# Kernel tuning notes

Hardware: AMD Instinct MI355X
Metric: run time of the kernel (lower is better)

The kernel has to match this reference:

```python
import jax, jax.numpy as jnp
import numpy as np
import math

N_EMBD = 1024
N_HEAD = 16
HEAD_SIZE = N_EMBD // N_HEAD
LAYER_IDX = 2
LAMBDA_INIT = 0.8 - 0.6 * math.exp(-0.3 * (LAYER_IDX - 1))
LN_EPS = 1e-5
B, T = 4, 1024


def setup_inputs() -> dict:
    key = jax.random.key(0)
    ks = jax.random.split(key, 11)
    s = 0.02  # weight init scale
    return {
        "x": jax.random.normal(ks[0], (B, T, N_EMBD), dtype=jnp.float32),
        "Wq1": jax.random.normal(ks[1], (N_EMBD, N_EMBD), dtype=jnp.float32) * s,
        "Wq2": jax.random.normal(ks[2], (N_EMBD, N_EMBD), dtype=jnp.float32) * s,
        "Wk1": jax.random.normal(ks[3], (N_EMBD, N_EMBD), dtype=jnp.float32) * s,
        "Wk2": jax.random.normal(ks[4], (N_EMBD, N_EMBD), dtype=jnp.float32) * s,
        "Wv": jax.random.normal(ks[5], (N_EMBD, 2 * N_EMBD), dtype=jnp.float32) * s,
        "Wc": jax.random.normal(ks[6], (2 * N_EMBD, N_EMBD), dtype=jnp.float32) * s,
        "lq1": jax.random.normal(ks[7], (N_HEAD, HEAD_SIZE), dtype=jnp.float32) * 0.1,
        "lk1": jax.random.normal(ks[8], (N_HEAD, HEAD_SIZE), dtype=jnp.float32) * 0.1,
        "lq2": jax.random.normal(ks[9], (N_HEAD, HEAD_SIZE), dtype=jnp.float32) * 0.1,
        "lk2": jax.random.normal(ks[10], (N_HEAD, HEAD_SIZE), dtype=jnp.float32) * 0.1,
    }


def reference(x, Wq1, Wq2, Wk1, Wk2, Wv, Wc, lq1, lk1, lq2, lk2):
    Bx, Tx, C = x.shape
    H, hs = N_HEAD, HEAD_SIZE
    scale = 1.0 / math.sqrt(hs)

    # projections -> (B, T, H, d)
    q1 = (x @ Wq1).reshape(Bx, Tx, H, hs)
    q2 = (x @ Wq2).reshape(Bx, Tx, H, hs)
    k1 = (x @ Wk1).reshape(Bx, Tx, H, hs)
    k2 = (x @ Wk2).reshape(Bx, Tx, H, hs)
    v = (x @ Wv).reshape(Bx, Tx, H, 2 * hs)

    # dual score streams (B, H, T, T)
    att1 = jnp.einsum("bqhd,bkhd->bhqk", q1, k1) * scale
    att2 = jnp.einsum("bqhd,bkhd->bhqk", q2, k2) * scale

    causal = jnp.tril(jnp.ones((Tx, Tx), dtype=bool))  # (T, T)
    neg_inf = jnp.float32(-jnp.inf)
    att1 = jnp.where(causal, att1, neg_inf)
    att2 = jnp.where(causal, att2, neg_inf)
    a1 = jax.nn.softmax(att1, axis=-1)
    a2 = jax.nn.softmax(att2, axis=-1)

    # per-head differential lambda
    lam1 = jnp.exp(jnp.sum(lq1 * lk1, axis=-1))  # (H,)
    lam2 = jnp.exp(jnp.sum(lq2 * lk2, axis=-1))  # (H,)
    lam_full = lam1 - lam2 + LAMBDA_INIT  # (H,)

    att = a1 - lam_full[None, :, None, None] * a2  # dropout = identity (eval)

    # PV matmul -> (B, T, H, 2*hs)
    y = jnp.einsum("bhqk,bkhd->bqhd", att, v)

    # subLN over last dim (no affine)
    mu = jnp.mean(y, axis=-1, keepdims=True)
    var = jnp.mean(jnp.square(y - mu), axis=-1, keepdims=True)
    y = (y - mu) / jnp.sqrt(var + LN_EPS)
    y = y * (1.0 - LAMBDA_INIT)

    y = y.reshape(Bx, Tx, 2 * C)
    return y @ Wc  # resid dropout = identity (eval)
```

## Files before the change

### kernel.cpp

```cpp
#include <hip/hip_runtime.h>


#define T_SEQ 1024
#define NH 16
#define DV 128
#define NPROJ 6144
#define KSTR 72

typedef __bf16 bf16_t;
typedef __bf16 bf16x8 __attribute__((ext_vector_type(8)));
typedef __bf16 bf16x4 __attribute__((ext_vector_type(4)));
typedef short s16x4 __attribute__((ext_vector_type(4)));
typedef float f32x4 __attribute__((ext_vector_type(4)));

#define LAMBDA_INIT 0.35550906759096928f
#define ONE_MINUS_LI 0.6444909324090307f
#define LOG2E 1.4426950408889634f
#define RTHR 44.36f

#if __has_builtin(__builtin_amdgcn_mfma_f32_16x16x16_bf16)
#define MFMA16(a, b, c) __builtin_amdgcn_mfma_f32_16x16x16_bf16(a, b, c, 0, 0, 0)
#elif __has_builtin(__builtin_amdgcn_mfma_f32_16x16x16bf16_1k)
#define MFMA16(a, b, c)                                                       \
  __builtin_amdgcn_mfma_f32_16x16x16bf16_1k(                                  \
      __builtin_bit_cast(s16x4, a), __builtin_bit_cast(s16x4, b), c, 0, 0, 0)
#else
#define MFMA16(a, b, c) (c)
#endif

#define GLDS(g, l)                                                            \
  __builtin_amdgcn_global_load_lds(                                           \
      (const __attribute__((address_space(1))) void*)(g),                     \
      (__attribute__((address_space(3))) void*)(l), 16, 0, 0)

static const size_t OFF_WCAT = 0;
static const size_t OFF_XB = OFF_WCAT + (size_t)6144 * 1024 * 2;
static const size_t OFF_WCT = OFF_XB + (size_t)4096 * 1024 * 2;
static const size_t OFF_PROJ = OFF_WCT + (size_t)2048 * 1024 * 2;
static const size_t OFF_VT = OFF_PROJ + (size_t)4096 * 6144 * 2;
static const size_t OFF_YLN = OFF_VT + (size_t)64 * 128 * 1024 * 2;
static const size_t OFF_LAM = OFF_YLN + (size_t)4096 * 2048 * 2;

__global__ void __launch_bounds__(256) cast_x(const float* __restrict__ x,
                                              bf16_t* __restrict__ o) {
  const int i = (blockIdx.x * 256 + threadIdx.x) * 4;
  float4 v = *(const float4*)(x + i);
  bf16x4 r = {(bf16_t)v.x, (bf16_t)v.y, (bf16_t)v.z, (bf16_t)v.w};
  *(bf16x4*)(o + i) = r;
}

__device__ __forceinline__ void tcast_body(const float* __restrict__ W,
                                           bf16_t* __restrict__ Wt, int K,
                                           int N, int row0) {
  __shared__ float tile[32][33];
  const int k0 = blockIdx.x * 32, n0 = blockIdx.y * 32;
  const int tx = threadIdx.x & 31, ty = threadIdx.x >> 5;
#pragma unroll
  for (int i = 0; i < 32; i += 8)
    tile[ty + i][tx] = W[(long)(k0 + ty + i) * N + n0 + tx];
  __syncthreads();
#pragma unroll
  for (int i = 0; i < 32; i += 8)
    Wt[(long)(row0 + n0 + ty + i) * K + k0 + tx] = (bf16_t)tile[tx][ty + i];
}

__global__ void __launch_bounds__(256) tcast_w(const float* __restrict__ W,
                                               bf16_t* __restrict__ Wt, int K,
                                               int N, int row0) {
  tcast_body(W, Wt, K, N, row0);
}

__global__ void __launch_bounds__(256) tcast_w4(const float* __restrict__ W0,
                                                const float* __restrict__ W1,
                                                const float* __restrict__ W2,
                                                const float* __restrict__ W3,
                                                bf16_t* __restrict__ Wt) {
  const float* Ws[4] = {W0, W1, W2, W3};
  tcast_body(Ws[blockIdx.z], Wt, 1024, 1024, blockIdx.z * 1024);
}

__global__ void lam_kernel(const float* __restrict__ lq1,
                           const float* __restrict__ lk1,
                           const float* __restrict__ lq2,
                           const float* __restrict__ lk2,
                           float* __restrict__ lam) {
  const int h = threadIdx.x;
  if (h < NH) {
    float d1 = 0.f, d2 = 0.f;
    for (int i = 0; i < 64; ++i) {
      d1 += lq1[h * 64 + i] * lk1[h * 64 + i];
      d2 += lq2[h * 64 + i] * lk2[h * 64 + i];
    }
    lam[h] = expf(d1) - expf(d2) + LAMBDA_INIT;
  }
}

#define BM 128
#define BN 128
#define BK 32

template <typename OutT>
__global__ void __launch_bounds__(256) gemm_bt(const bf16_t* __restrict__ A,
                                               const bf16_t* __restrict__ Bt,
                                               OutT* __restrict__ C, int M,
                                               int N, int K) {
  __shared__ __align__(16) bf16_t As[BM * BK];
  __shared__ __align__(16) bf16_t Bs[BN * BK];
  const int tid = threadIdx.x;
  const int w = tid >> 6;
  const int lane = tid & 63;
  const int quad = lane >> 4, l16 = lane & 15;
  const int m0 = blockIdx.y * BM, n0 = blockIdx.x * BN;
  const int wm = (w >> 1) * 64, wn = (w & 1) * 64;
  const int srow = tid >> 2;
  const int scol = (tid & 3) * 8;

  const bf16_t* Ag0 = A + (long)(m0 + srow) * K + scol;
  const bf16_t* Ag1 = Ag0 + (long)64 * K;
  const bf16_t* Bg0 = Bt + (long)(n0 + srow) * K + scol;
  const bf16_t* Bg1 = Bg0 + (long)64 * K;
  bf16_t* lA0 = As + tid * 8;
  bf16_t* lA1 = As + 2048 + tid * 8;
  bf16_t* lB0 = Bs + tid * 8;
  bf16_t* lB1 = Bs + 2048 + tid * 8;

  f32x4 acc[4][4] = {};

  for (int k0 = 0; k0 < K; k0 += BK) {
    GLDS(Ag0 + k0, lA0);
    GLDS(Ag1 + k0, lA1);
    GLDS(Bg0 + k0, lB0);
    GLDS(Bg1 + k0, lB1);
    __syncthreads();
    bf16x8 af[4], bfr[4];
#pragma unroll
    for (int t = 0; t < 4; ++t) {
      af[t] = *(const bf16x8*)(As + (wm + t * 16 + l16) * BK + quad * 8);
      bfr[t] = *(const bf16x8*)(Bs + (wn + t * 16 + l16) * BK + quad * 8);
    }
#pragma unroll
    for (int mt = 0; mt < 4; ++mt)
#pragma unroll
      for (int nt = 0; nt < 4; ++nt)
        acc[mt][nt] = __builtin_amdgcn_mfma_f32_16x16x32_bf16(
            af[mt], bfr[nt], acc[mt][nt], 0, 0, 0);
    __syncthreads();
  }

#pragma unroll
  for (int mt = 0; mt < 4; ++mt)
#pragma unroll
    for (int nt = 0; nt < 4; ++nt) {
      const int col = n0 + wn + nt * 16 + l16;
#pragma unroll
      for (int i = 0; i < 4; ++i) {
        const int row = m0 + wm + mt * 16 + quad * 4 + i;
        C[(long)row * N + col] = (OutT)acc[mt][nt][i];
      }
    }
}

__global__ void __launch_bounds__(256) transpose_v(const bf16_t* __restrict__ proj,
                                                   bf16_t* __restrict__ vt) {
  __shared__ bf16_t tile[32][34];
  const int bh = blockIdx.z;
  const int b = bh >> 4, h = bh & 15;
  const int t0 = blockIdx.x * 32, d0 = blockIdx.y * 32;
  const int tx = threadIdx.x & 31, ty = threadIdx.x >> 5;
  const bf16_t* src = proj + (long)(b * T_SEQ) * NPROJ + 4096 + h * 128;
#pragma unroll
  for (int i = 0; i < 32; i += 8)
    tile[ty + i][tx] = src[(long)(t0 + ty + i) * NPROJ + d0 + tx];
  __syncthreads();
  bf16_t* dst = vt + ((long)(b * NH + h) * DV) * T_SEQ;
#pragma unroll
  for (int i = 0; i < 32; i += 8)
    dst[(long)(d0 + ty + i) * T_SEQ + t0 + tx] = tile[tx][ty + i];
}

__global__ void __launch_bounds__(256) attn_kernel(const bf16_t* __restrict__ proj,
                                                   const bf16_t* __restrict__ vt,
                                                   const float* __restrict__ lamp,
                                                   bf16_t* __restrict__ yln) {
  const int x = blockIdx.x;
  const int qblk = 15 - (x >> 6);
  const int bh = x & 63;
  const int b = bh >> 4, h = bh & 15;
  const int tid = threadIdx.x;
  const int w = tid >> 6, lane = tid & 63;
  const int quad = lane >> 4, l16 = lane & 15;
  const long bT = (long)b * T_SEQ;

  __shared__ __align__(16) bf16_t Ks1[64 * KSTR];
  __shared__ __align__(16) bf16_t Ks2[64 * KSTR];
  __shared__ __align__(16) bf16_t Vs[DV * KSTR];

  const bf16_t* gK1 =
      proj + (bT + (tid >> 3)) * (long)NPROJ + h * 64 + 2048 + (tid & 7) * 8;
  const bf16_t* gK2 = gK1 + 1024;
  const bf16_t* vbase = vt + ((long)(b * NH + h) * DV) * T_SEQ;
  const bf16_t* gV = vbase + (long)(tid >> 3) * T_SEQ + (tid & 7) * 8;
  const int kw0 = (tid >> 3) * KSTR + (tid & 7) * 8;

  const float sc = 0.125f * LOG2E;
  const float lam = lamp[h];

  const int q0 = qblk * 64 + w * 16;
  const int qg = q0 + l16;

  const bf16_t* qrow = proj + (bT + qg) * (long)NPROJ + h * 64;
  bf16x8 aq1[2], aq2[2];
  aq1[0] = *(const bf16x8*)(qrow + quad * 8);
  aq1[1] = *(const bf16x8*)(qrow + 32 + quad * 8);
  aq2[0] = *(const bf16x8*)(qrow + 1024 + quad * 8);
  aq2[1] = *(const bf16x8*)(qrow + 1024 + 32 + quad * 8);

  f32x4 O1[8] = {}, O2[8] = {};
  float m1 = -3.0e38f, m2 = -3.0e38f, l1 = 0.f, l2 = 0.f;

  const int kend_blk = qblk * 64 + 64;
  const int kend_w = q0 + 16;

  const bf16x4 one4 = {(bf16_t)1.0f, (bf16_t)1.0f, (bf16_t)1.0f, (bf16_t)1.0f};

  bf16x8 rK1[2], rK2[2], rV[4];
  rK1[0] = *(const bf16x8*)(gK1);
  rK1[1] = *(const bf16x8*)(gK1 + (long)32 * NPROJ);
  rK2[0] = *(const bf16x8*)(gK2);
  rK2[1] = *(const bf16x8*)(gK2 + (long)32 * NPROJ);
#pragma unroll
  for (int j = 0; j < 4; ++j)
    rV[j] = *(const bf16x8*)(gV + (long)(32 * j) * T_SEQ);

  for (int kt = 0; kt < kend_blk; kt += 64) {
    *(bf16x8*)(Ks1 + kw0) = rK1[0];
    *(bf16x8*)(Ks1 + kw0 + 32 * KSTR) = rK1[1];
    *(bf16x8*)(Ks2 + kw0) = rK2[0];
    *(bf16x8*)(Ks2 + kw0 + 32 * KSTR) = rK2[1];
#pragma unroll
    for (int j = 0; j < 4; ++j)
      *(bf16x8*)(Vs + kw0 + j * 32 * KSTR) = rV[j];
    __syncthreads();

    if (kt + 64 < kend_blk) {
      const long ko = (long)(kt + 64) * NPROJ;
      rK1[0] = *(const bf16x8*)(gK1 + ko);
      rK1[1] = *(const bf16x8*)(gK1 + ko + (long)32 * NPROJ);
      rK2[0] = *(const bf16x8*)(gK2 + ko);
      rK2[1] = *(const bf16x8*)(gK2 + ko + (long)32 * NPROJ);
#pragma unroll
      for (int j = 0; j < 4; ++j)
        rV[j] = *(const bf16x8*)(gV + kt + 64 + (long)(32 * j) * T_SEQ);
    }

    if (kt < kend_w) {
      f32x4 s1[4], s2[4];
#pragma unroll
      for (int c = 0; c < 4; ++c) {
        const bf16_t* kr1 = Ks1 + (c * 16 + l16) * KSTR;
        const bf16_t* kr2 = Ks2 + (c * 16 + l16) * KSTR;
        bf16x8 ka0 = *(const bf16x8*)(kr1 + quad * 8);
        bf16x8 ka1 = *(const bf16x8*)(kr1 + 32 + quad * 8);
        f32x4 z = {};
        z = __builtin_amdgcn_mfma_f32_16x16x32_bf16(ka0, aq1[0], z, 0, 0, 0);
        z = __builtin_amdgcn_mfma_f32_16x16x32_bf16(ka1, aq1[1], z, 0, 0, 0);
        s1[c] = z;
        bf16x8 kb0 = *(const bf16x8*)(kr2 + quad * 8);
        bf16x8 kb1 = *(const bf16x8*)(kr2 + 32 + quad * 8);
        f32x4 z2 = {};
        z2 = __builtin_amdgcn_mfma_f32_16x16x32_bf16(kb0, aq2[0], z2, 0, 0, 0);
        z2 = __builtin_amdgcn_mfma_f32_16x16x32_bf16(kb1, aq2[1], z2, 0, 0, 0);
        s2[c] = z2;
      }
      const bool need_mask = (kt + 63 > q0);
      if (need_mask) {
#pragma unroll
        for (int c = 0; c < 4; ++c)
#pragma unroll
          for (int i = 0; i < 4; ++i) {
            const int key = kt + c * 16 + quad * 4 + i;
            if (key > qg) {
              s1[c][i] = -1e30f;
              s2[c][i] = -1e30f;
            }
          }
      }
      float t1[4], t2[4];
#pragma unroll
      for (int c = 0; c < 4; ++c) {
        t1[c] = fmaxf(fmaxf(s1[c][0], s1[c][1]), fmaxf(s1[c][2], s1[c][3]));
        t2[c] = fmaxf(fmaxf(s2[c][0], s2[c][1]), fmaxf(s2[c][2], s2[c][3]));
      }
      float mx1 = fmaxf(fmaxf(t1[0], t1[1]), fmaxf(t1[2], t1[3]));
      float mx2 = fmaxf(fmaxf(t2[0], t2[1]), fmaxf(t2[2], t2[3]));
      mx1 = fmaxf(mx1, __shfl_xor(mx1, 16));
      mx1 = fmaxf(mx1, __shfl_xor(mx1, 32));
      mx2 = fmaxf(mx2, __shfl_xor(mx2, 16));
      mx2 = fmaxf(mx2, __shfl_xor(mx2, 32));
      if (!__all((mx1 <= m1 + RTHR) && (mx2 <= m2 + RTHR))) {
        const float mn1 = fmaxf(m1, mx1), mn2 = fmaxf(m2, mx2);
        const float al1 = exp2f((m1 - mn1) * sc);
        const float al2 = exp2f((m2 - mn2) * sc);
        m1 = mn1;
        m2 = mn2;
#pragma unroll
        for (int f = 0; f < 8; ++f)
#pragma unroll
          for (int i = 0; i < 4; ++i) {
            O1[f][i] *= al1;
            O2[f][i] *= al2;
          }
        l1 *= al1;
        l2 *= al2;
      }
      const float ms1 = m1 * sc, ms2 = m2 * sc;
      bf16x4 pc1[4], pc2[4];
#pragma unroll
      for (int c = 0; c < 4; ++c)
#pragma unroll
        for (int i = 0; i < 4; ++i) {
          pc1[c][i] = (bf16_t)exp2f(fmaf(s1[c][i], sc, -ms1));
          pc2[c][i] = (bf16_t)exp2f(fmaf(s2[c][i], sc, -ms2));
        }
      f32x4 la1 = {}, la2 = {};
#pragma unroll
      for (int c = 0; c < 4; ++c) {
        la1 = MFMA16(one4, pc1[c], la1);
        la2 = MFMA16(one4, pc2[c], la2);
#pragma unroll
        for (int f = 0; f < 8; ++f) {
          bf16x4 va =
              *(const bf16x4*)(Vs + (f * 16 + l16) * KSTR + c * 16 + quad * 4);
          O1[f] = MFMA16(va, pc1[c], O1[f]);
          O2[f] = MFMA16(va, pc2[c], O2[f]);
        }
      }
      l1 += la1[0];
      l2 += la2[0];
    }
    __syncthreads();
  }

  const float inv1 = 1.0f / l1, inv2 = lam / l2;
  float sm = 0.f, sq = 0.f;
#pragma unroll
  for (int f = 0; f < 8; ++f)
#pragma unroll
    for (int i = 0; i < 4; ++i) {
      float y = O1[f][i] * inv1 - O2[f][i] * inv2;
      O1[f][i] = y;
      sm += y;
      sq += y * y;
    }
  sm += __shfl_xor(sm, 16);
  sm += __shfl_xor(sm, 32);
  sq += __shfl_xor(sq, 16);
  sq += __shfl_xor(sq, 32);
  const float mu = sm * (1.0f / 128.0f);
  const float var = sq * (1.0f / 128.0f) - mu * mu;
  const float rs = rsqrtf(var + 1e-5f) * ONE_MINUS_LI;
  bf16_t* dst = yln + (bT + qg) * (long)2048 + h * 128 + quad * 4;
#pragma unroll
  for (int f = 0; f < 8; ++f) {
    bf16x4 o = {(bf16_t)((O1[f][0] - mu) * rs), (bf16_t)((O1[f][1] - mu) * rs),
                (bf16_t)((O1[f][2] - mu) * rs), (bf16_t)((O1[f][3] - mu) * rs)};
    *(bf16x4*)(dst + f * 16) = o;
  }
}

extern "C" void kernel_launch(void* const* d_in, const int* in_sizes, int n_in,
                              void* d_out, int out_size, void* d_ws,
                              size_t ws_size, hipStream_t stream) {
  const float* x = (const float*)d_in[0];
  const float* Wq1 = (const float*)d_in[1];
  const float* Wq2 = (const float*)d_in[2];
  const float* Wk1 = (const float*)d_in[3];
  const float* Wk2 = (const float*)d_in[4];
  const float* Wv = (const float*)d_in[5];
  const float* Wc = (const float*)d_in[6];
  const float* lq1 = (const float*)d_in[7];
  const float* lk1 = (const float*)d_in[8];
  const float* lq2 = (const float*)d_in[9];
  const float* lk2 = (const float*)d_in[10];
  float* out = (float*)d_out;

  char* ws = (char*)d_ws;
  bf16_t* wcat = (bf16_t*)(ws + OFF_WCAT);
  bf16_t* xb = (bf16_t*)(ws + OFF_XB);
  bf16_t* wct = (bf16_t*)(ws + OFF_WCT);
  bf16_t* projb = (bf16_t*)(ws + OFF_PROJ);
  bf16_t* vtb = (bf16_t*)(ws + OFF_VT);
  bf16_t* ylnb = (bf16_t*)(ws + OFF_YLN);
  float* lamp = (float*)(ws + OFF_LAM);

  cast_x<<<4096, 256, 0, stream>>>(x, xb);
  tcast_w4<<<dim3(32, 32, 4), 256, 0, stream>>>(Wq1, Wq2, Wk1, Wk2, wcat);
  tcast_w<<<dim3(32, 64), 256, 0, stream>>>(Wv, wcat, 1024, 2048, 4096);
  tcast_w<<<dim3(64, 32), 256, 0, stream>>>(Wc, wct, 2048, 1024, 0);
  lam_kernel<<<1, 64, 0, stream>>>(lq1, lk1, lq2, lk2, lamp);

  gemm_bt<bf16_t><<<dim3(48, 32), 256, 0, stream>>>(xb, wcat, projb, 4096, 6144, 1024);
  transpose_v<<<dim3(32, 4, 64), 256, 0, stream>>>(projb, vtb);
  attn_kernel<<<dim3(1024), 256, 0, stream>>>(projb, vtb, lamp, ylnb);
  gemm_bt<float><<<dim3(8, 32), 256, 0, stream>>>(ylnb, wct, out, 4096, 1024, 2048);
}
```

Baseline: 334.3 us.

## Drop LDS staging in attention; single-wave blocks read K/V directly from global

The attention kernel now runs one 64-thread wave per block instead of four waves sharing LDS tiles. Each wave loads K and V fragments straight from global memory into registers. The block index is remapped so heads are grouped per XCD and share L2, and the wave stops at its own causal limit rather than the block's. To allow 16-byte V loads that split into two MFMA operands, transpose_v writes V^T with keys interleaved in that order. This removes LDS traffic, barriers and idle waves on the diagonal, at the cost of more global/L2 loads, since each wave re-reads K/V without sharing.

```diff
diff --git a/kernel.cpp b/kernel.cpp
--- a/kernel.cpp
+++ b/kernel.cpp
@@ -5,7 +5,6 @@
 #define NH 16
 #define DV 128
 #define NPROJ 6144
-#define KSTR 72
 
 typedef __bf16 bf16_t;
 typedef __bf16 bf16x8 __attribute__((ext_vector_type(8)));
@@ -172,39 +171,36 @@
   for (int i = 0; i < 32; i += 8)
     tile[ty + i][tx] = src[(long)(t0 + ty + i) * NPROJ + d0 + tx];
   __syncthreads();
-  bf16_t* dst = vt + ((long)(b * NH + h) * DV) * T_SEQ;
-#pragma unroll
-  for (int i = 0; i < 32; i += 8)
-    dst[(long)(d0 + ty + i) * T_SEQ + t0 + tx] = tile[tx][ty + i];
-}
-
-__global__ void __launch_bounds__(256) attn_kernel(const bf16_t* __restrict__ proj,
-                                                   const bf16_t* __restrict__ vt,
-                                                   const float* __restrict__ lamp,
-                                                   bf16_t* __restrict__ yln) {
+  const int d_loc = threadIdx.x >> 3;
+  const int g = threadIdx.x & 7;
+  const int s = g >> 2, qd = g & 3;
+  const int tl = s * 16 + qd * 4;
+  bf16x4 o = {tile[tl + 0][d_loc], tile[tl + 1][d_loc], tile[tl + 2][d_loc],
+              tile[tl + 3][d_loc]};
+  bf16_t* dst = vt + (long)bh * (DV * T_SEQ) + (long)(d0 + d_loc) * T_SEQ;
+  *(bf16x4*)(dst + t0 + qd * 8 + s * 4) = o;
+}
+
+__global__ void __launch_bounds__(64, 3) attn_kernel(const bf16_t* __restrict__ proj,
+                                                     const bf16_t* __restrict__ vt,
+                                                     const float* __restrict__ lamp,
+                                                     bf16_t* __restrict__ yln) {
   const int x = blockIdx.x;
-  const int qblk = 15 - (x >> 6);
-  const int bh = x & 63;
+  const int xcd = x & 7;
+  const int u = x >> 3;
+  const int p2 = u >> 7, r = u & 127;
+  const int qi = r >> 3;
+  const int bhl = p2 * 2 + ((r >> 2) & 1);
+  const int w = r & 3;
+  const int qblk = 15 - qi;
+  const int bh = (bhl << 3) | xcd;
   const int b = bh >> 4, h = bh & 15;
-  const int tid = threadIdx.x;
-  const int w = tid >> 6, lane = tid & 63;
+  const int lane = threadIdx.x;
   const int quad = lane >> 4, l16 = lane & 15;
   const long bT = (long)b * T_SEQ;
 
-  __shared__ __align__(16) bf16_t Ks1[64 * KSTR];
-  __shared__ __align__(16) bf16_t Ks2[64 * KSTR];
-  __shared__ __align__(16) bf16_t Vs[DV * KSTR];
-
-  const bf16_t* gK1 =
-      proj + (bT + (tid >> 3)) * (long)NPROJ + h * 64 + 2048 + (tid & 7) * 8;
-  const bf16_t* gK2 = gK1 + 1024;
-  const bf16_t* vbase = vt + ((long)(b * NH + h) * DV) * T_SEQ;
-  const bf16_t* gV = vbase + (long)(tid >> 3) * T_SEQ + (tid & 7) * 8;
-  const int kw0 = (tid >> 3) * KSTR + (tid & 7) * 8;
-
   const float sc = 0.125f * LOG2E;
   const float lam = lamp[h];
-
   const int q0 = qblk * 64 + w * 16;
   const int qg = q0 + l16;
 
@@ -215,130 +211,104 @@
   aq2[0] = *(const bf16x8*)(qrow + 1024 + quad * 8);
   aq2[1] = *(const bf16x8*)(qrow + 1024 + 32 + quad * 8);
 
+  const bf16_t* kb = proj + (bT + l16) * (long)NPROJ + h * 64 + 2048 + quad * 8;
+  const bf16_t* vb = vt + (long)bh * (DV * T_SEQ) + (long)l16 * T_SEQ + quad * 8;
+
   f32x4 O1[8] = {}, O2[8] = {};
   float m1 = -3.0e38f, m2 = -3.0e38f, l1 = 0.f, l2 = 0.f;
-
-  const int kend_blk = qblk * 64 + 64;
-  const int kend_w = q0 + 16;
-
   const bf16x4 one4 = {(bf16_t)1.0f, (bf16_t)1.0f, (bf16_t)1.0f, (bf16_t)1.0f};
 
-  bf16x8 rK1[2], rK2[2], rV[4];
-  rK1[0] = *(const bf16x8*)(gK1);
-  rK1[1] = *(const bf16x8*)(gK1 + (long)32 * NPROJ);
-  rK2[0] = *(const bf16x8*)(gK2);
-  rK2[1] = *(const bf16x8*)(gK2 + (long)32 * NPROJ);
-#pragma unroll
-  for (int j = 0; j < 4; ++j)
-    rV[j] = *(const bf16x8*)(gV + (long)(32 * j) * T_SEQ);
-
-  for (int kt = 0; kt < kend_blk; kt += 64) {
-    *(bf16x8*)(Ks1 + kw0) = rK1[0];
-    *(bf16x8*)(Ks1 + kw0 + 32 * KSTR) = rK1[1];
-    *(bf16x8*)(Ks2 + kw0) = rK2[0];
-    *(bf16x8*)(Ks2 + kw0 + 32 * KSTR) = rK2[1];
-#pragma unroll
-    for (int j = 0; j < 4; ++j)
-      *(bf16x8*)(Vs + kw0 + j * 32 * KSTR) = rV[j];
-    __syncthreads();
-
-    if (kt + 64 < kend_blk) {
-      const long ko = (long)(kt + 64) * NPROJ;
-      rK1[0] = *(const bf16x8*)(gK1 + ko);
-      rK1[1] = *(const bf16x8*)(gK1 + ko + (long)32 * NPROJ);
-      rK2[0] = *(const bf16x8*)(gK2 + ko);
-      rK2[1] = *(const bf16x8*)(gK2 + ko + (long)32 * NPROJ);
-#pragma unroll
-      for (int j = 0; j < 4; ++j)
-        rV[j] = *(const bf16x8*)(gV + kt + 64 + (long)(32 * j) * T_SEQ);
-    }
-
-    if (kt < kend_w) {
-      f32x4 s1[4], s2[4];
-#pragma unroll
-      for (int c = 0; c < 4; ++c) {
-        const bf16_t* kr1 = Ks1 + (c * 16 + l16) * KSTR;
-        const bf16_t* kr2 = Ks2 + (c * 16 + l16) * KSTR;
-        bf16x8 ka0 = *(const bf16x8*)(kr1 + quad * 8);
-        bf16x8 ka1 = *(const bf16x8*)(kr1 + 32 + quad * 8);
-        f32x4 z = {};
-        z = __builtin_amdgcn_mfma_f32_16x16x32_bf16(ka0, aq1[0], z, 0, 0, 0);
-        z = __builtin_amdgcn_mfma_f32_16x16x32_bf16(ka1, aq1[1], z, 0, 0, 0);
-        s1[c] = z;
-        bf16x8 kb0 = *(const bf16x8*)(kr2 + quad * 8);
-        bf16x8 kb1 = *(const bf16x8*)(kr2 + 32 + quad * 8);
-        f32x4 z2 = {};
-        z2 = __builtin_amdgcn_mfma_f32_16x16x32_bf16(kb0, aq2[0], z2, 0, 0, 0);
-        z2 = __builtin_amdgcn_mfma_f32_16x16x32_bf16(kb1, aq2[1], z2, 0, 0, 0);
-        s2[c] = z2;
+  const int kend = q0 + 16;
+  for (int kt = 0; kt < kend; kt += 64) {
+    f32x4 s1[4], s2[4];
+#pragma unroll
+    for (int c = 0; c < 4; ++c) {
+      const bf16_t* kp = kb + (long)(kt + c * 16) * NPROJ;
+      bf16x8 ka0 = *(const bf16x8*)(kp);
+      bf16x8 ka1 = *(const bf16x8*)(kp + 32);
+      bf16x8 kb0 = *(const bf16x8*)(kp + 1024);
+      bf16x8 kb1 = *(const bf16x8*)(kp + 1056);
+      f32x4 z = {};
+      z = __builtin_amdgcn_mfma_f32_16x16x32_bf16(ka0, aq1[0], z, 0, 0, 0);
+      z = __builtin_amdgcn_mfma_f32_16x16x32_bf16(ka1, aq1[1], z, 0, 0, 0);
+      s1[c] = z;
+      f32x4 z2 = {};
+      z2 = __builtin_amdgcn_mfma_f32_16x16x32_bf16(kb0, aq2[0], z2, 0, 0, 0);
+      z2 = __builtin_amdgcn_mfma_f32_16x16x32_bf16(kb1, aq2[1], z2, 0, 0, 0);
+      s2[c] = z2;
+    }
+    const bool need_mask = (kt + 63 > q0);
+    if (need_mask) {
+#pragma unroll
+      for (int c = 0; c < 4; ++c)
+#pragma unroll
+        for (int i = 0; i < 4; ++i) {
+          const int key = kt + c * 16 + quad * 4 + i;
+          if (key > qg) {
+            s1[c][i] = -1e30f;
+            s2[c][i] = -1e30f;
+          }
+        }
+    }
+    float t1[4], t2[4];
+#pragma unroll
+    for (int c = 0; c < 4; ++c) {
+      t1[c] = fmaxf(fmaxf(s1[c][0], s1[c][1]), fmaxf(s1[c][2], s1[c][3]));
+      t2[c] = fmaxf(fmaxf(s2[c][0], s2[c][1]), fmaxf(s2[c][2], s2[c][3]));
+    }
+    float mx1 = fmaxf(fmaxf(t1[0], t1[1]), fmaxf(t1[2], t1[3]));
+    float mx2 = fmaxf(fmaxf(t2[0], t2[1]), fmaxf(t2[2], t2[3]));
+    mx1 = fmaxf(mx1, __shfl_xor(mx1, 16));
+    mx1 = fmaxf(mx1, __shfl_xor(mx1, 32));
+    mx2 = fmaxf(mx2, __shfl_xor(mx2, 16));
+    mx2 = fmaxf(mx2, __shfl_xor(mx2, 32));
+    if (!__all((mx1 <= m1 + RTHR) && (mx2 <= m2 + RTHR))) {
+      const float mn1 = fmaxf(m1, mx1), mn2 = fmaxf(m2, mx2);
+      const float al1 = exp2f((m1 - mn1) * sc);
+      const float al2 = exp2f((m2 - mn2) * sc);
+      m1 = mn1;
+      m2 = mn2;
+#pragma unroll
+      for (int f = 0; f < 8; ++f)
+#pragma unroll
+        for (int i = 0; i < 4; ++i) {
+          O1[f][i] *= al1;
+          O2[f][i] *= al2;
+        }
+      l1 *= al1;
+      l2 *= al2;
+    }
+    const float ms1 = m1 * sc, ms2 = m2 * sc;
+    bf16x4 pc1[4], pc2[4];
+#pragma unroll
+    for (int c = 0; c < 4; ++c)
+#pragma unroll
+      for (int i = 0; i < 4; ++i) {
+        pc1[c][i] = (bf16_t)exp2f(fmaf(s1[c][i], sc, -ms1));
+        pc2[c][i] = (bf16_t)exp2f(fmaf(s2[c][i], sc, -ms2));
       }
-      const bool need_mask = (kt + 63 > q0);
-      if (need_mask) {
-#pragma unroll
-        for (int c = 0; c < 4; ++c)
-#pragma unroll
-          for (int i = 0; i < 4; ++i) {
-            const int key = kt + c * 16 + quad * 4 + i;
-            if (key > qg) {
-              s1[c][i] = -1e30f;
-              s2[c][i] = -1e30f;
-            }
-          }
+    f32x4 la1 = {}, la2 = {};
+#pragma unroll
+    for (int c = 0; c < 4; ++c) {
+      la1 = MFMA16(one4, pc1[c], la1);
+      la2 = MFMA16(one4, pc2[c], la2);
+    }
+#pragma unroll
+    for (int cp = 0; cp < 2; ++cp) {
+      const bf16_t* vp = vb + kt + cp * 32;
+#pragma unroll
+      for (int f = 0; f < 8; ++f) {
+        bf16x8 va = *(const bf16x8*)(vp + (long)f * 16 * T_SEQ);
+        bf16x4 lo = __builtin_shufflevector(va, va, 0, 1, 2, 3);
+        bf16x4 hi = __builtin_shufflevector(va, va, 4, 5, 6, 7);
+        O1[f] = MFMA16(lo, pc1[2 * cp], O1[f]);
+        O2[f] = MFMA16(lo, pc2[2 * cp], O2[f]);
+        O1[f] = MFMA16(hi, pc1[2 * cp + 1], O1[f]);
+        O2[f] = MFMA16(hi, pc2[2 * cp + 1], O2[f]);
       }
-      float t1[4], t2[4];
-#pragma unroll
-      for (int c = 0; c < 4; ++c) {
-        t1[c] = fmaxf(fmaxf(s1[c][0], s1[c][1]), fmaxf(s1[c][2], s1[c][3]));
-        t2[c] = fmaxf(fmaxf(s2[c][0], s2[c][1]), fmaxf(s2[c][2], s2[c][3]));
-      }
-      float mx1 = fmaxf(fmaxf(t1[0], t1[1]), fmaxf(t1[2], t1[3]));
-      float mx2 = fmaxf(fmaxf(t2[0], t2[1]), fmaxf(t2[2], t2[3]));
-      mx1 = fmaxf(mx1, __shfl_xor(mx1, 16));
-      mx1 = fmaxf(mx1, __shfl_xor(mx1, 32));
-      mx2 = fmaxf(mx2, __shfl_xor(mx2, 16));
-      mx2 = fmaxf(mx2, __shfl_xor(mx2, 32));
-      if (!__all((mx1 <= m1 + RTHR) && (mx2 <= m2 + RTHR))) {
-        const float mn1 = fmaxf(m1, mx1), mn2 = fmaxf(m2, mx2);
-        const float al1 = exp2f((m1 - mn1) * sc);
-        const float al2 = exp2f((m2 - mn2) * sc);
-        m1 = mn1;
-        m2 = mn2;
-#pragma unroll
-        for (int f = 0; f < 8; ++f)
-#pragma unroll
-          for (int i = 0; i < 4; ++i) {
-            O1[f][i] *= al1;
-            O2[f][i] *= al2;
-          }
-        l1 *= al1;
-        l2 *= al2;
-      }
-      const float ms1 = m1 * sc, ms2 = m2 * sc;
-      bf16x4 pc1[4], pc2[4];
-#pragma unroll
-      for (int c = 0; c < 4; ++c)
-#pragma unroll
-        for (int i = 0; i < 4; ++i) {
-          pc1[c][i] = (bf16_t)exp2f(fmaf(s1[c][i], sc, -ms1));
-          pc2[c][i] = (bf16_t)exp2f(fmaf(s2[c][i], sc, -ms2));
-        }
-      f32x4 la1 = {}, la2 = {};
-#pragma unroll
-      for (int c = 0; c < 4; ++c) {
-        la1 = MFMA16(one4, pc1[c], la1);
-        la2 = MFMA16(one4, pc2[c], la2);
-#pragma unroll
-        for (int f = 0; f < 8; ++f) {
-          bf16x4 va =
-              *(const bf16x4*)(Vs + (f * 16 + l16) * KSTR + c * 16 + quad * 4);
-          O1[f] = MFMA16(va, pc1[c], O1[f]);
-          O2[f] = MFMA16(va, pc2[c], O2[f]);
-        }
-      }
-      l1 += la1[0];
-      l2 += la2[0];
-    }
-    __syncthreads();
+    }
+    l1 += la1[0];
+    l2 += la2[0];
   }
 
   const float inv1 = 1.0f / l1, inv2 = lam / l2;
@@ -401,6 +371,6 @@
 
   gemm_bt<bf16_t><<<dim3(48, 32), 256, 0, stream>>>(xb, wcat, projb, 4096, 6144, 1024);
   transpose_v<<<dim3(32, 4, 64), 256, 0, stream>>>(projb, vtb);
-  attn_kernel<<<dim3(1024), 256, 0, stream>>>(projb, vtb, lamp, ylnb);
+  attn_kernel<<<dim3(4096), 64, 0, stream>>>(projb, vtb, lamp, ylnb);
   gemm_bt<float><<<dim3(8, 32), 256, 0, stream>>>(ylnb, wct, out, 4096, 1024, 2048);
 }
```

Measured after the change: 397.0 us. +18.7%, slower.

## Split dual attention streams into separate blocks, add combine kernel and narrower output GEMM

Applied to the files above, without the earlier changes.

The attention kernel now computes each softmax stream (q1/k1 and q2/k2) in its own block, doubling the grid to 2048 blocks. Each block writes a normalized fp16 partial output. A new combine kernel applies lambda, the subLN and the scale, reusing the workspace regions of yln and wcat. The final projection uses a new 64-wide N tile GEMM, which launches twice as many blocks. This raises parallelism and lowers per-block register pressure, at the cost of V tiles being loaded twice, fp16 round trips through memory and an extra kernel launch.

```diff
diff --git a/kernel.cpp b/kernel.cpp
--- a/kernel.cpp
+++ b/kernel.cpp
@@ -10,6 +10,9 @@
 typedef __bf16 bf16_t;
 typedef __bf16 bf16x8 __attribute__((ext_vector_type(8)));
 typedef __bf16 bf16x4 __attribute__((ext_vector_type(4)));
+typedef __bf16 bf16x2 __attribute__((ext_vector_type(2)));
+typedef _Float16 f16x4 __attribute__((ext_vector_type(4)));
+typedef _Float16 f16x2 __attribute__((ext_vector_type(2)));
 typedef short s16x4 __attribute__((ext_vector_type(4)));
 typedef float f32x4 __attribute__((ext_vector_type(4)));
 
@@ -160,6 +163,65 @@
     }
 }
 
+template <typename OutT>
+__global__ void __launch_bounds__(256) gemm_bt_n64(const bf16_t* __restrict__ A,
+                                                   const bf16_t* __restrict__ Bt,
+                                                   OutT* __restrict__ C, int M,
+                                                   int N, int K) {
+  __shared__ __align__(16) bf16_t As[BM * BK];
+  __shared__ __align__(16) bf16_t Bs[64 * BK];
+  const int tid = threadIdx.x;
+  const int w = tid >> 6;
+  const int lane = tid & 63;
+  const int quad = lane >> 4, l16 = lane & 15;
+  const int m0 = blockIdx.y * BM, n0 = blockIdx.x * 64;
+  const int wm = (w >> 1) * 64, wn = (w & 1) * 32;
+  const int srow = tid >> 2;
+  const int scol = (tid & 3) * 8;
+
+  const bf16_t* Ag0 = A + (long)(m0 + srow) * K + scol;
+  const bf16_t* Ag1 = Ag0 + (long)64 * K;
+  const bf16_t* Bg0 = Bt + (long)(n0 + srow) * K + scol;
+  bf16_t* lA0 = As + tid * 8;
+  bf16_t* lA1 = As + 2048 + tid * 8;
+  bf16_t* lB0 = Bs + tid * 8;
+
+  f32x4 acc[4][2] = {};
+
+  for (int k0 = 0; k0 < K; k0 += BK) {
+    GLDS(Ag0 + k0, lA0);
+    GLDS(Ag1 + k0, lA1);
+    GLDS(Bg0 + k0, lB0);
+    __syncthreads();
+    bf16x8 af[4], bfr[2];
+#pragma unroll
+    for (int t = 0; t < 4; ++t)
+      af[t] = *(const bf16x8*)(As + (wm + t * 16 + l16) * BK + quad * 8);
+#pragma unroll
+    for (int t = 0; t < 2; ++t)
+      bfr[t] = *(const bf16x8*)(Bs + (wn + t * 16 + l16) * BK + quad * 8);
+#pragma unroll
+    for (int mt = 0; mt < 4; ++mt)
+#pragma unroll
+      for (int nt = 0; nt < 2; ++nt)
+        acc[mt][nt] = __builtin_amdgcn_mfma_f32_16x16x32_bf16(
+            af[mt], bfr[nt], acc[mt][nt], 0, 0, 0);
+    __syncthreads();
+  }
+
+#pragma unroll
+  for (int mt = 0; mt < 4; ++mt)
+#pragma unroll
+    for (int nt = 0; nt < 2; ++nt) {
+      const int col = n0 + wn + nt * 16 + l16;
+#pragma unroll
+      for (int i = 0; i < 4; ++i) {
+        const int row = m0 + wm + mt * 16 + quad * 4 + i;
+        C[(long)row * N + col] = (OutT)acc[mt][nt][i];
+      }
+    }
+}
+
 __global__ void __launch_bounds__(256) transpose_v(const bf16_t* __restrict__ proj,
                                                    bf16_t* __restrict__ vt) {
   __shared__ bf16_t tile[32][34];
@@ -172,7 +234,7 @@
   for (int i = 0; i < 32; i += 8)
     tile[ty + i][tx] = src[(long)(t0 + ty + i) * NPROJ + d0 + tx];
   __syncthreads();
-  bf16_t* dst = vt + ((long)(b * NH + h) * DV) * T_SEQ;
+  bf16_t* dst = vt + ((long)bh * DV) * T_SEQ;
 #pragma unroll
   for (int i = 0; i < 32; i += 8)
     dst[(long)(d0 + ty + i) * T_SEQ + t0 + tx] = tile[tx][ty + i];
@@ -180,10 +242,11 @@
 
 __global__ void __launch_bounds__(256) attn_kernel(const bf16_t* __restrict__ proj,
                                                    const bf16_t* __restrict__ vt,
-                                                   const float* __restrict__ lamp,
-                                                   bf16_t* __restrict__ yln) {
+                                                   _Float16* __restrict__ a1,
+                                                   _Float16* __restrict__ a2) {
   const int x = blockIdx.x;
-  const int qblk = 15 - (x >> 6);
+  const int qblk = 15 - (x >> 7);
+  const int st = (x >> 6) & 1;
   const int bh = x & 63;
   const int b = bh >> 4, h = bh & 15;
   const int tid = threadIdx.x;
@@ -191,181 +254,150 @@
   const int quad = lane >> 4, l16 = lane & 15;
   const long bT = (long)b * T_SEQ;
 
-  __shared__ __align__(16) bf16_t Ks1[64 * KSTR];
-  __shared__ __align__(16) bf16_t Ks2[64 * KSTR];
+  __shared__ __align__(16) bf16_t Ks[64 * KSTR];
   __shared__ __align__(16) bf16_t Vs[DV * KSTR];
 
-  const bf16_t* gK1 =
-      proj + (bT + (tid >> 3)) * (long)NPROJ + h * 64 + 2048 + (tid & 7) * 8;
-  const bf16_t* gK2 = gK1 + 1024;
-  const bf16_t* vbase = vt + ((long)(b * NH + h) * DV) * T_SEQ;
-  const bf16_t* gV = vbase + (long)(tid >> 3) * T_SEQ + (tid & 7) * 8;
-  const int kw0 = (tid >> 3) * KSTR + (tid & 7) * 8;
+  const int koff = h * 64 + 2048 + st * 1024;
+  const bf16_t* gK = proj + (bT + (tid >> 2)) * (long)NPROJ + koff + (tid & 3) * 16;
+  const bf16_t* gV = vt + (long)bh * DV * T_SEQ + (long)(tid >> 1) * T_SEQ +
+                     (tid & 1) * 32;
+  const int kwK = (tid >> 2) * KSTR + (tid & 3) * 16;
+  const int kwV = (tid >> 1) * KSTR + (tid & 1) * 32;
 
   const float sc = 0.125f * LOG2E;
-  const float lam = lamp[h];
-
   const int q0 = qblk * 64 + w * 16;
   const int qg = q0 + l16;
 
-  const bf16_t* qrow = proj + (bT + qg) * (long)NPROJ + h * 64;
-  bf16x8 aq1[2], aq2[2];
-  aq1[0] = *(const bf16x8*)(qrow + quad * 8);
-  aq1[1] = *(const bf16x8*)(qrow + 32 + quad * 8);
-  aq2[0] = *(const bf16x8*)(qrow + 1024 + quad * 8);
-  aq2[1] = *(const bf16x8*)(qrow + 1024 + 32 + quad * 8);
-
-  f32x4 O1[8] = {}, O2[8] = {};
-  float m1 = -3.0e38f, m2 = -3.0e38f, l1 = 0.f, l2 = 0.f;
+  const bf16_t* qrow = proj + (bT + qg) * (long)NPROJ + h * 64 + st * 1024;
+  bf16x8 aq[2];
+  aq[0] = *(const bf16x8*)(qrow + quad * 8);
+  aq[1] = *(const bf16x8*)(qrow + 32 + quad * 8);
+
+  f32x4 O[8] = {};
+  float m = -3.0e38f, l = 0.f;
+  const bf16x4 one4 = {(bf16_t)1.0f, (bf16_t)1.0f, (bf16_t)1.0f, (bf16_t)1.0f};
 
   const int kend_blk = qblk * 64 + 64;
   const int kend_w = q0 + 16;
 
-  const bf16x4 one4 = {(bf16_t)1.0f, (bf16_t)1.0f, (bf16_t)1.0f, (bf16_t)1.0f};
-
-  bf16x8 rK1[2], rK2[2], rV[4];
-  rK1[0] = *(const bf16x8*)(gK1);
-  rK1[1] = *(const bf16x8*)(gK1 + (long)32 * NPROJ);
-  rK2[0] = *(const bf16x8*)(gK2);
-  rK2[1] = *(const bf16x8*)(gK2 + (long)32 * NPROJ);
-#pragma unroll
-  for (int j = 0; j < 4; ++j)
-    rV[j] = *(const bf16x8*)(gV + (long)(32 * j) * T_SEQ);
+  bf16x8 rK[2], rV[4];
+  rK[0] = *(const bf16x8*)(gK);
+  rK[1] = *(const bf16x8*)(gK + 8);
+#pragma unroll
+  for (int j = 0; j < 4; ++j) rV[j] = *(const bf16x8*)(gV + j * 8);
 
   for (int kt = 0; kt < kend_blk; kt += 64) {
-    *(bf16x8*)(Ks1 + kw0) = rK1[0];
-    *(bf16x8*)(Ks1 + kw0 + 32 * KSTR) = rK1[1];
-    *(bf16x8*)(Ks2 + kw0) = rK2[0];
-    *(bf16x8*)(Ks2 + kw0 + 32 * KSTR) = rK2[1];
-#pragma unroll
-    for (int j = 0; j < 4; ++j)
-      *(bf16x8*)(Vs + kw0 + j * 32 * KSTR) = rV[j];
+    *(bf16x8*)(Ks + kwK) = rK[0];
+    *(bf16x8*)(Ks + kwK + 8) = rK[1];
+#pragma unroll
+    for (int j = 0; j < 4; ++j) *(bf16x8*)(Vs + kwV + j * 8) = rV[j];
     __syncthreads();
 
     if (kt + 64 < kend_blk) {
       const long ko = (long)(kt + 64) * NPROJ;
-      rK1[0] = *(const bf16x8*)(gK1 + ko);
-      rK1[1] = *(const bf16x8*)(gK1 + ko + (long)32 * NPROJ);
-      rK2[0] = *(const bf16x8*)(gK2 + ko);
-      rK2[1] = *(const bf16x8*)(gK2 + ko + (long)32 * NPROJ);
+      rK[0] = *(const bf16x8*)(gK + ko);
+      rK[1] = *(const bf16x8*)(gK + ko + 8);
 #pragma unroll
       for (int j = 0; j < 4; ++j)
-        rV[j] = *(const bf16x8*)(gV + kt + 64 + (long)(32 * j) * T_SEQ);
+        rV[j] = *(const bf16x8*)(gV + kt + 64 + j * 8);
     }
 
     if (kt < kend_w) {
-      f32x4 s1[4], s2[4];
+      f32x4 s[4];
 #pragma unroll
       for (int c = 0; c < 4; ++c) {
-        const bf16_t* kr1 = Ks1 + (c * 16 + l16) * KSTR;
-        const bf16_t* kr2 = Ks2 + (c * 16 + l16) * KSTR;
-        bf16x8 ka0 = *(const bf16x8*)(kr1 + quad * 8);
-        bf16x8 ka1 = *(const bf16x8*)(kr1 + 32 + quad * 8);
+        const bf16_t* kr = Ks + (c * 16 + l16) * KSTR;
+        bf16x8 ka0 = *(const bf16x8*)(kr + quad * 8);
+        bf16x8 ka1 = *(const bf16x8*)(kr + 32 + quad * 8);
         f32x4 z = {};
-        z = __builtin_amdgcn_mfma_f32_16x16x32_bf16(ka0, aq1[0], z, 0, 0, 0);
-        z = __builtin_amdgcn_mfma_f32_16x16x32_bf16(ka1, aq1[1], z, 0, 0, 0);
-        s1[c] = z;
-        bf16x8 kb0 = *(const bf16x8*)(kr2 + quad * 8);
-        bf16x8 kb1 = *(const bf16x8*)(kr2 + 32 + quad * 8);
-        f32x4 z2 = {};
-        z2 = __builtin_amdgcn_mfma_f32_16x16x32_bf16(kb0, aq2[0], z2, 0, 0, 0);
-        z2 = __builtin_amdgcn_mfma_f32_16x16x32_bf16(kb1, aq2[1], z2, 0, 0, 0);
-        s2[c] = z2;
-      }
-      const bool need_mask = (kt + 63 > q0);
-      if (need_mask) {
+        z = __builtin_amdgcn_mfma_f32_16x16x32_bf16(ka0, aq[0], z, 0, 0, 0);
+        z = __builtin_amdgcn_mfma_f32_16x16x32_bf16(ka1, aq[1], z, 0, 0, 0);
+        s[c] = z;
+      }
+      if (kt + 63 > q0) {
 #pragma unroll
         for (int c = 0; c < 4; ++c)
 #pragma unroll
           for (int i = 0; i < 4; ++i) {
             const int key = kt + c * 16 + quad * 4 + i;
-            if (key > qg) {
-              s1[c][i] = -1e30f;
-              s2[c][i] = -1e30f;
-            }
+            if (key > qg) s[c][i] = -1e30f;
           }
       }
-      float t1[4], t2[4];
+      float t[4];
+#pragma unroll
+      for (int c = 0; c < 4; ++c)
+        t[c] = fmaxf(fmaxf(s[c][0], s[c][1]), fmaxf(s[c][2], s[c][3]));
+      float mx = fmaxf(fmaxf(t[0], t[1]), fmaxf(t[2], t[3]));
+      mx = fmaxf(mx, __shfl_xor(mx, 16));
+      mx = fmaxf(mx, __shfl_xor(mx, 32));
+      if (!__all(mx <= m + RTHR)) {
+        const float mn = fmaxf(m, mx);
+        const float al = exp2f((m - mn) * sc);
+        m = mn;
+#pragma unroll
+        for (int f = 0; f < 8; ++f)
+#pragma unroll
+          for (int i = 0; i < 4; ++i) O[f][i] *= al;
+        l *= al;
+      }
+      const float ms = m * sc;
+      bf16x4 pc[4];
+#pragma unroll
+      for (int c = 0; c < 4; ++c)
+#pragma unroll
+        for (int i = 0; i < 4; ++i)
+          pc[c][i] = (bf16_t)exp2f(fmaf(s[c][i], sc, -ms));
+      f32x4 la = {};
+#pragma unroll
+      for (int c = 0; c < 4; ++c) la = MFMA16(one4, pc[c], la);
 #pragma unroll
       for (int c = 0; c < 4; ++c) {
-        t1[c] = fmaxf(fmaxf(s1[c][0], s1[c][1]), fmaxf(s1[c][2], s1[c][3]));
-        t2[c] = fmaxf(fmaxf(s2[c][0], s2[c][1]), fmaxf(s2[c][2], s2[c][3]));
-      }
-      float mx1 = fmaxf(fmaxf(t1[0], t1[1]), fmaxf(t1[2], t1[3]));
-      float mx2 = fmaxf(fmaxf(t2[0], t2[1]), fmaxf(t2[2], t2[3]));
-      mx1 = fmaxf(mx1, __shfl_xor(mx1, 16));
-      mx1 = fmaxf(mx1, __shfl_xor(mx1, 32));
-      mx2 = fmaxf(mx2, __shfl_xor(mx2, 16));
-      mx2 = fmaxf(mx2, __shfl_xor(mx2, 32));
-      if (!__all((mx1 <= m1 + RTHR) && (mx2 <= m2 + RTHR))) {
-        const float mn1 = fmaxf(m1, mx1), mn2 = fmaxf(m2, mx2);
-        const float al1 = exp2f((m1 - mn1) * sc);
-        const float al2 = exp2f((m2 - mn2) * sc);
-        m1 = mn1;
-        m2 = mn2;
-#pragma unroll
-        for (int f = 0; f < 8; ++f)
-#pragma unroll
-          for (int i = 0; i < 4; ++i) {
-            O1[f][i] *= al1;
-            O2[f][i] *= al2;
-          }
-        l1 *= al1;
-        l2 *= al2;
-      }
-      const float ms1 = m1 * sc, ms2 = m2 * sc;
-      bf16x4 pc1[4], pc2[4];
-#pragma unroll
-      for (int c = 0; c < 4; ++c)
-#pragma unroll
-        for (int i = 0; i < 4; ++i) {
-          pc1[c][i] = (bf16_t)exp2f(fmaf(s1[c][i], sc, -ms1));
-          pc2[c][i] = (bf16_t)exp2f(fmaf(s2[c][i], sc, -ms2));
-        }
-      f32x4 la1 = {}, la2 = {};
-#pragma unroll
-      for (int c = 0; c < 4; ++c) {
-        la1 = MFMA16(one4, pc1[c], la1);
-        la2 = MFMA16(one4, pc2[c], la2);
 #pragma unroll
         for (int f = 0; f < 8; ++f) {
           bf16x4 va =
               *(const bf16x4*)(Vs + (f * 16 + l16) * KSTR + c * 16 + quad * 4);
-          O1[f] = MFMA16(va, pc1[c], O1[f]);
-          O2[f] = MFMA16(va, pc2[c], O2[f]);
+          O[f] = MFMA16(va, pc[c], O[f]);
         }
       }
-      l1 += la1[0];
-      l2 += la2[0];
-    }
-    __syncthreads();
-  }
-
-  const float inv1 = 1.0f / l1, inv2 = lam / l2;
-  float sm = 0.f, sq = 0.f;
-#pragma unroll
-  for (int f = 0; f < 8; ++f)
-#pragma unroll
-    for (int i = 0; i < 4; ++i) {
-      float y = O1[f][i] * inv1 - O2[f][i] * inv2;
-      O1[f][i] = y;
-      sm += y;
-      sq += y * y;
-    }
-  sm += __shfl_xor(sm, 16);
-  sm += __shfl_xor(sm, 32);
-  sq += __shfl_xor(sq, 16);
-  sq += __shfl_xor(sq, 32);
+      l += la[0];
+    }
+    __syncthreads();
+  }
+
+  const float inv = 1.0f / l;
+  _Float16* ob = st ? a2 : a1;
+  _Float16* dst = ob + ((bT + qg) * 16 + h) * (long)128 + quad * 4;
+#pragma unroll
+  for (int f = 0; f < 8; ++f) {
+    f16x4 o = {(_Float16)(O[f][0] * inv), (_Float16)(O[f][1] * inv),
+               (_Float16)(O[f][2] * inv), (_Float16)(O[f][3] * inv)};
+    *(f16x4*)(dst + f * 16) = o;
+  }
+}
+
+__global__ void __launch_bounds__(256) combine_kernel(const _Float16* __restrict__ a1,
+                                                      const _Float16* __restrict__ a2,
+                                                      const float* __restrict__ lamp,
+                                                      bf16_t* __restrict__ yln) {
+  const int unit = blockIdx.x * 4 + (threadIdx.x >> 6);
+  const int lane = threadIdx.x & 63;
+  const float lam = lamp[unit & 15];
+  const long base = (long)unit * 128 + lane * 2;
+  f16x2 v1 = *(const f16x2*)(a1 + base);
+  f16x2 v2 = *(const f16x2*)(a2 + base);
+  float y0 = (float)v1[0] - lam * (float)v2[0];
+  float y1 = (float)v1[1] - lam * (float)v2[1];
+  float sm = y0 + y1, sq = y0 * y0 + y1 * y1;
+#pragma unroll
+  for (int off = 1; off < 64; off <<= 1) {
+    sm += __shfl_xor(sm, off);
+    sq += __shfl_xor(sq, off);
+  }
   const float mu = sm * (1.0f / 128.0f);
   const float var = sq * (1.0f / 128.0f) - mu * mu;
   const float rs = rsqrtf(var + 1e-5f) * ONE_MINUS_LI;
-  bf16_t* dst = yln + (bT + qg) * (long)2048 + h * 128 + quad * 4;
-#pragma unroll
-  for (int f = 0; f < 8; ++f) {
-    bf16x4 o = {(bf16_t)((O1[f][0] - mu) * rs), (bf16_t)((O1[f][1] - mu) * rs),
-                (bf16_t)((O1[f][2] - mu) * rs), (bf16_t)((O1[f][3] - mu) * rs)};
-    *(bf16x4*)(dst + f * 16) = o;
-  }
+  bf16x2 o = {(bf16_t)((y0 - mu) * rs), (bf16_t)((y1 - mu) * rs)};
+  *(bf16x2*)(yln + base) = o;
 }
 
 extern "C" void kernel_launch(void* const* d_in, const int* in_sizes, int n_in,
@@ -392,6 +424,8 @@
   bf16_t* vtb = (bf16_t*)(ws + OFF_VT);
   bf16_t* ylnb = (bf16_t*)(ws + OFF_YLN);
   float* lamp = (float*)(ws + OFF_LAM);
+  _Float16* a1b = (_Float16*)(ws + OFF_YLN);
+  _Float16* a2b = (_Float16*)(ws + OFF_WCAT);
 
   cast_x<<<4096, 256, 0, stream>>>(x, xb);
   tcast_w4<<<dim3(32, 32, 4), 256, 0, stream>>>(Wq1, Wq2, Wk1, Wk2, wcat);
@@ -401,6 +435,7 @@
 
   gemm_bt<bf16_t><<<dim3(48, 32), 256, 0, stream>>>(xb, wcat, projb, 4096, 6144, 1024);
   transpose_v<<<dim3(32, 4, 64), 256, 0, stream>>>(projb, vtb);
-  attn_kernel<<<dim3(1024), 256, 0, stream>>>(projb, vtb, lamp, ylnb);
-  gemm_bt<float><<<dim3(8, 32), 256, 0, stream>>>(ylnb, wct, out, 4096, 1024, 2048);
-}
+  attn_kernel<<<dim3(2048), 256, 0, stream>>>(projb, vtb, a1b, a2b);
+  combine_kernel<<<dim3(16384), 256, 0, stream>>>(a1b, a2b, lamp, ylnb);
+  gemm_bt_n64<float><<<dim3(16, 32), 256, 0, stream>>>(ylnb, wct, out, 4096, 1024, 2048);
+}
```

New measurement: 308.6 us. 7.7% less time.
